# Kernel optimization log

Measured on AMD Instinct MI355X. Metric: run time of the kernel, lower is better.

Reference implementation:

```python
import jax, jax.numpy as jnp
import numpy as np


def setup_inputs() -> dict:
    key = jax.random.key(0)
    ks = jax.random.split(key, 7)
    B, N, D, A = 32, 128, 512, 512
    sD = 1.0 / np.sqrt(D)
    sA = 1.0 / np.sqrt(A)
    return {
        "x": jax.random.normal(ks[0], (B, N, D), dtype=jnp.float32),
        "W1": jax.random.normal(ks[1], (A, D), dtype=jnp.float32) * sD,
        "b1": jax.random.normal(ks[2], (A,), dtype=jnp.float32) * sD,
        "W2": jax.random.normal(ks[3], (A, D), dtype=jnp.float32) * sD,
        "b2": jax.random.normal(ks[4], (A,), dtype=jnp.float32) * sD,
        "Wout": jax.random.normal(ks[5], (A,), dtype=jnp.float32) * sA,
        "bout": jax.random.normal(ks[6], (1,), dtype=jnp.float32) * sA,
    }


def reference(x, W1, b1, W2, b2, Wout, bout):
    # x: (B, N, D)
    x1 = jnp.einsum('bnd,ad->bna', x, W1) + b1  # mlp1 -> (B, N, A)
    x2 = jnp.einsum('bnd,ad->bna', x, W2) + b2  # mlp2 -> (B, N, A)
    # outer broadcast add: x1.unsqueeze(1) + x2.unsqueeze(2) -> (B, N, N, A)
    s = x1[:, None, :, :] + x2[:, :, None, :]
    # include_root=False: drop ROOT row along dim 1 -> (B, N-1, N, A)
    s = s[:, 1:, :, :]
    s = jnp.tanh(s)
    # out linear A -> 1, then squeeze -> (B, N-1, N)
    return jnp.einsum('bija,a->bij', s, Wout) + bout[0]
```

## Files before the change

kernel.cpp:

```cpp
#include <hip/hip_runtime.h>
#include <hip/hip_bf16.h>

#define B_ 32
#define N_ 128
#define D_ 512
#define A_ 512
#define R_ (B_*N_)
#define OC 1024
#define CEXP 2.8853900817779268f

typedef __attribute__((ext_vector_type(8))) short  frag_ab;
typedef __attribute__((ext_vector_type(4))) float  frag_cd;

__device__ inline unsigned pack2bf(float a, float b) {
    unsigned ua = __builtin_bit_cast(unsigned, a) + 0x8000u;
    unsigned ub = __builtin_bit_cast(unsigned, b) + 0x8000u;
    return __builtin_amdgcn_perm(ub, ua, 0x07060302);
}
__device__ inline float bf2f_lo(unsigned u){ return __builtin_bit_cast(float, u << 16); }
__device__ inline float bf2f_hi(unsigned u){ return __builtin_bit_cast(float, u & 0xffff0000u); }

__global__ __launch_bounds__(256) void k0_cvt(
    const float* __restrict__ X, const float* __restrict__ W1,
    const float* __restrict__ W2,
    unsigned short* __restrict__ Xb, unsigned short* __restrict__ W1b,
    unsigned short* __restrict__ W2b)
{
    const int NX = R_*D_/8, NW = A_*D_/8;
    int i = blockIdx.x*256 + threadIdx.x;
    const float* src; unsigned short* dst; int off;
    if (i < NX)            { src = X;  dst = Xb;  off = i; }
    else if (i < NX+NW)    { src = W1; dst = W1b; off = i-NX; }
    else if (i < NX+2*NW)  { src = W2; dst = W2b; off = i-NX-NW; }
    else return;
    float4 a = ((const float4*)src)[off*2];
    float4 c = ((const float4*)src)[off*2+1];
    uint4 o;
    o.x = pack2bf(a.x,a.y); o.y = pack2bf(a.z,a.w);
    o.z = pack2bf(c.x,c.y); o.w = pack2bf(c.z,c.w);
    ((uint4*)dst)[off] = o;
}

#define BK1 64
#define LDK 68

__global__ __launch_bounds__(256) void k1_mfma(
    const unsigned short* __restrict__ Xb,
    const unsigned short* __restrict__ W1b, const float* __restrict__ b1,
    const unsigned short* __restrict__ W2b, const float* __restrict__ b2,
    unsigned short* __restrict__ Yb)
{
    __shared__ unsigned short As[2][64*LDK];
    __shared__ unsigned short Bs[2][64*LDK];

    const int t = threadIdx.x, lane = t&63, wid = t>>6;
    const int wr = wid>>1, wc = wid&1;
    const int row0 = blockIdx.x*64, col0 = blockIdx.y*64;
    const unsigned short* Wb = (col0 < A_) ? W1b : W2b;
    const float* bb = (col0 < A_) ? b1 : b2;
    const int wrow0 = col0 & (A_-1);

    const int srow = t>>3;
    const int scol = (t&7)*8;

    frag_cd acc[2][2];
#pragma unroll
    for (int i=0;i<2;++i)
#pragma unroll
        for (int j=0;j<2;++j) acc[i][j] = frag_cd{0.f,0.f,0.f,0.f};

    const int fr = lane&15, g8 = (lane>>4)*8;

    uint4 ra[2], rb[2];
#pragma unroll
    for (int q=0;q<2;++q){
        int r = q*32 + srow;
        ra[q] = *(const uint4*)&Xb[(size_t)(row0 +r)*D_ + scol];
        rb[q] = *(const uint4*)&Wb[(size_t)(wrow0+r)*D_ + scol];
    }
#pragma unroll
    for (int q=0;q<2;++q){
        int r = q*32 + srow;
        *(uint4*)&As[0][r*LDK + scol] = ra[q];
        *(uint4*)&Bs[0][r*LDK + scol] = rb[q];
    }
    __syncthreads();

#pragma unroll
    for (int s=0; s<8; ++s) {
        const int cur = s&1;
        if (s<7) {
            const int k0 = (s+1)*BK1;
#pragma unroll
            for (int q=0;q<2;++q){
                int r = q*32 + srow;
                ra[q] = *(const uint4*)&Xb[(size_t)(row0 +r)*D_ + k0 + scol];
                rb[q] = *(const uint4*)&Wb[(size_t)(wrow0+r)*D_ + k0 + scol];
            }
        }
        frag_ab af[2][2], bf[2][2];
#pragma unroll
        for (int fi=0;fi<2;++fi)
#pragma unroll
            for (int ks=0;ks<2;++ks) {
                af[fi][ks] = *(const frag_ab*)&As[cur][(wr*32+fi*16+fr)*LDK + ks*32 + g8];
                bf[fi][ks] = *(const frag_ab*)&Bs[cur][(wc*32+fi*16+fr)*LDK + ks*32 + g8];
            }
#pragma unroll
        for (int ks=0;ks<2;++ks)
#pragma unroll
            for (int fi=0;fi<2;++fi)
#pragma unroll
                for (int fj=0;fj<2;++fj)
                    acc[fi][fj] = __builtin_amdgcn_mfma_f32_16x16x32_bf16(
                        af[fi][ks], bf[fj][ks], acc[fi][fj], 0, 0, 0);
        if (s<7) {
#pragma unroll
            for (int q=0;q<2;++q){
                int r = q*32 + srow;
                *(uint4*)&As[cur^1][r*LDK + scol] = ra[q];
                *(uint4*)&Bs[cur^1][r*LDK + scol] = rb[q];
            }
        }
        __syncthreads();
    }

#pragma unroll
    for (int fi=0;fi<2;++fi){
        const int rr = row0 + wr*32 + fi*16 + (lane>>4)*4;
#pragma unroll
        for (int fj=0;fj<2;++fj){
            const int cc = col0 + wc*32 + fj*16 + (lane&15);
            const float bias = bb[cc & (A_-1)];
#pragma unroll
            for (int r=0;r<4;++r){
                float e = __builtin_amdgcn_exp2f(CEXP*(acc[fi][fj][r] + bias));
                Yb[(size_t)(rr+r)*OC + cc] =
                    (unsigned short)((__builtin_bit_cast(unsigned, e) + 0x8000u) >> 16);
            }
        }
    }
}

#define ACH 128
#define LDA2 (ACH+4)

__global__ __launch_bounds__(256) void k2_tanh(
    const unsigned short* __restrict__ Yb,
    const float* __restrict__ Wout, const float* __restrict__ bout,
    float* __restrict__ out)
{
    __shared__ float e1s[32][LDA2];
    __shared__ float e2s[16][LDA2];
    __shared__ float wo[A_];
    __shared__ float wsum_s[4];

    const int t  = threadIdx.x;
    const int jt = blockIdx.x;
    const int it = blockIdx.y;
    const int b  = blockIdx.z;

    float wsacc = 0.f;
    for (int k=t; k<A_; k+=256){ float w = Wout[k]; wo[k] = w; wsacc += w; }
#pragma unroll
    for (int off=32; off>=1; off>>=1) wsacc += __shfl_down(wsacc, off, 64);
    if ((t&63)==0) wsum_s[t>>6] = wsacc;

    const unsigned short* yb = Yb + (size_t)b*N_*OC;
    const int sr = t>>4;
    const int sc = (t&15)*8;

    uint4 p1a = *(const uint4*)&yb[(size_t)(jt*32 + sr     )*OC + sc];
    uint4 p1b = *(const uint4*)&yb[(size_t)(jt*32 + sr + 16)*OC + sc];
    int i2c = it*16 + sr + 1; if (i2c > 127) i2c = 127;
    uint4 p2  = *(const uint4*)&yb[(size_t)i2c*OC + A_ + sc];
    {
        uint4 v = p1a;
        *(float4*)&e1s[sr][sc]   = float4{bf2f_lo(v.x),bf2f_hi(v.x),bf2f_lo(v.y),bf2f_hi(v.y)};
        *(float4*)&e1s[sr][sc+4] = float4{bf2f_lo(v.z),bf2f_hi(v.z),bf2f_lo(v.w),bf2f_hi(v.w)};
        v = p1b;
        *(float4*)&e1s[sr+16][sc]   = float4{bf2f_lo(v.x),bf2f_hi(v.x),bf2f_lo(v.y),bf2f_hi(v.y)};
        *(float4*)&e1s[sr+16][sc+4] = float4{bf2f_lo(v.z),bf2f_hi(v.z),bf2f_lo(v.w),bf2f_hi(v.w)};
        v = p2;
        *(float4*)&e2s[sr][sc]   = float4{bf2f_lo(v.x),bf2f_hi(v.x),bf2f_lo(v.y),bf2f_hi(v.y)};
        *(float4*)&e2s[sr][sc+4] = float4{bf2f_lo(v.z),bf2f_hi(v.z),bf2f_lo(v.w),bf2f_hi(v.w)};
    }
    __syncthreads();

    const int jl = t&15, il = t>>4;
    float a00 = 0.f, a01 = 0.f;

#pragma unroll
    for (int ch=0; ch<4; ++ch) {
        if (ch<3) {
            const int a0n = (ch+1)*ACH;
            p1a = *(const uint4*)&yb[(size_t)(jt*32 + sr     )*OC + a0n + sc];
            p1b = *(const uint4*)&yb[(size_t)(jt*32 + sr + 16)*OC + a0n + sc];
            p2  = *(const uint4*)&yb[(size_t)i2c*OC + A_ + a0n + sc];
        }
        const int a0 = ch*ACH;
#pragma unroll 4
        for (int c=0; c<ACH; c+=4) {
            float4 u0 = *(const float4*)&e1s[jl     ][c];
            float4 u1 = *(const float4*)&e1s[jl + 16][c];
            float4 v0 = *(const float4*)&e2s[il     ][c];
            float4 w  = *(const float4*)&wo[a0 + c];
            a00 += w.x * __builtin_amdgcn_rcpf(fmaf(u0.x, v0.x, 1.f));
            a01 += w.x * __builtin_amdgcn_rcpf(fmaf(u1.x, v0.x, 1.f));
            a00 += w.y * __builtin_amdgcn_rcpf(fmaf(u0.y, v0.y, 1.f));
            a01 += w.y * __builtin_amdgcn_rcpf(fmaf(u1.y, v0.y, 1.f));
            a00 += w.z * __builtin_amdgcn_rcpf(fmaf(u0.z, v0.z, 1.f));
            a01 += w.z * __builtin_amdgcn_rcpf(fmaf(u1.z, v0.z, 1.f));
            a00 += w.w * __builtin_amdgcn_rcpf(fmaf(u0.w, v0.w, 1.f));
            a01 += w.w * __builtin_amdgcn_rcpf(fmaf(u1.w, v0.w, 1.f));
        }
        if (ch<3) {
            __syncthreads();
            uint4 v = p1a;
            *(float4*)&e1s[sr][sc]   = float4{bf2f_lo(v.x),bf2f_hi(v.x),bf2f_lo(v.y),bf2f_hi(v.y)};
            *(float4*)&e1s[sr][sc+4] = float4{bf2f_lo(v.z),bf2f_hi(v.z),bf2f_lo(v.w),bf2f_hi(v.w)};
            v = p1b;
            *(float4*)&e1s[sr+16][sc]   = float4{bf2f_lo(v.x),bf2f_hi(v.x),bf2f_lo(v.y),bf2f_hi(v.y)};
            *(float4*)&e1s[sr+16][sc+4] = float4{bf2f_lo(v.z),bf2f_hi(v.z),bf2f_lo(v.w),bf2f_hi(v.w)};
            v = p2;
            *(float4*)&e2s[sr][sc]   = float4{bf2f_lo(v.x),bf2f_hi(v.x),bf2f_lo(v.y),bf2f_hi(v.y)};
            *(float4*)&e2s[sr][sc+4] = float4{bf2f_lo(v.z),bf2f_hi(v.z),bf2f_lo(v.w),bf2f_hi(v.w)};
            __syncthreads();
        }
    }

    const float wsum = wsum_s[0] + wsum_s[1] + wsum_s[2] + wsum_s[3];
    const float bo   = bout[0];
    const int i0 = it*16 + il;
    const int j0 = jt*32 + jl;

    if (i0 < 127) {
        out[((size_t)(b*127) + i0) * 128 + j0     ] = wsum - 2.f*a00 + bo;
        out[((size_t)(b*127) + i0) * 128 + j0 + 16] = wsum - 2.f*a01 + bo;
    }
}

extern "C" void kernel_launch(void* const* d_in, const int* in_sizes, int n_in,
                              void* d_out, int out_size, void* d_ws, size_t ws_size,
                              hipStream_t stream) {
    const float* x    = (const float*)d_in[0];
    const float* W1   = (const float*)d_in[1];
    const float* b1   = (const float*)d_in[2];
    const float* W2   = (const float*)d_in[3];
    const float* b2   = (const float*)d_in[4];
    const float* Wout = (const float*)d_in[5];
    const float* bout = (const float*)d_in[6];
    float* out = (float*)d_out;

    char* ws = (char*)d_ws;
    unsigned short* Yb  = (unsigned short*)ws;
    unsigned short* Xb  = (unsigned short*)(ws + (8u<<20));
    unsigned short* W1b = (unsigned short*)(ws + (12u<<20));
    unsigned short* W2b = (unsigned short*)(ws + (12u<<20) + (1u<<19));

    k0_cvt<<<1280, 256, 0, stream>>>(x, W1, W2, Xb, W1b, W2b);

    dim3 g1(R_/64, OC/64);
    k1_mfma<<<g1, 256, 0, stream>>>(Xb, W1b, b1, W2b, b2, Yb);

    dim3 g2(4, 8, B_);
    k2_tanh<<<g2, 256, 0, stream>>>(Yb, Wout, bout, out);
}
```

Before: 115.6 us.

## Enlarge GEMM tiles to 32x32 MFMA and split tanh reduction across A halves

The projection GEMM moves from 64x64 tiles with 16x16x32 MFMA to 128x128 tiles with 32x32x16 MFMA and a K step of 32, raising data reuse per block. The tanh kernel now gives each thread a 2x2 output tile so loaded values are reused across more outputs. Pairs of reciprocals are merged into one rcp via the identity w1/r + w2/s = (w1*s + w2*r)/(r*s). The A dimension is split across two blocks whose partial sums are combined with atomicAdd into an output zeroed by a memset. This adds launch, memset and atomic overhead, makes float summation order nondeterministic, and the merged reciprocal risks overflow of r*s.

```diff
diff --git a/kernel.cpp b/kernel.cpp
--- a/kernel.cpp
+++ b/kernel.cpp
@@ -9,8 +9,8 @@
 #define OC 1024
 #define CEXP 2.8853900817779268f
 
-typedef __attribute__((ext_vector_type(8))) short  frag_ab;
-typedef __attribute__((ext_vector_type(4))) float  frag_cd;
+typedef __attribute__((ext_vector_type(8)))  short frag_ab;
+typedef __attribute__((ext_vector_type(16))) float frag_c;
 
 __device__ inline unsigned pack2bf(float a, float b) {
     unsigned ua = __builtin_bit_cast(unsigned, a) + 0x8000u;
@@ -19,6 +19,10 @@
 }
 __device__ inline float bf2f_lo(unsigned u){ return __builtin_bit_cast(float, u << 16); }
 __device__ inline float bf2f_hi(unsigned u){ return __builtin_bit_cast(float, u & 0xffff0000u); }
+__device__ inline void wr8(float* dst, uint4 v) {
+    *(float4*)dst     = float4{bf2f_lo(v.x),bf2f_hi(v.x),bf2f_lo(v.y),bf2f_hi(v.y)};
+    *(float4*)(dst+4) = float4{bf2f_lo(v.z),bf2f_hi(v.z),bf2f_lo(v.w),bf2f_hi(v.w)};
+}
 
 __global__ __launch_bounds__(256) void k0_cvt(
     const float* __restrict__ X, const float* __restrict__ W1,
@@ -41,8 +45,7 @@
     ((uint4*)dst)[off] = o;
 }
 
-#define BK1 64
-#define LDK 68
+#define LDK1 36
 
 __global__ __launch_bounds__(256) void k1_mfma(
     const unsigned short* __restrict__ Xb,
@@ -50,193 +53,198 @@
     const unsigned short* __restrict__ W2b, const float* __restrict__ b2,
     unsigned short* __restrict__ Yb)
 {
-    __shared__ unsigned short As[2][64*LDK];
-    __shared__ unsigned short Bs[2][64*LDK];
+    __shared__ unsigned short As[2][128*LDK1];
+    __shared__ unsigned short Bs[2][128*LDK1];
 
     const int t = threadIdx.x, lane = t&63, wid = t>>6;
     const int wr = wid>>1, wc = wid&1;
-    const int row0 = blockIdx.x*64, col0 = blockIdx.y*64;
+    const int row0 = blockIdx.x*128, col0 = blockIdx.y*128;
     const unsigned short* Wb = (col0 < A_) ? W1b : W2b;
     const float* bb = (col0 < A_) ? b1 : b2;
     const int wrow0 = col0 & (A_-1);
 
-    const int srow = t>>3;
-    const int scol = (t&7)*8;
-
-    frag_cd acc[2][2];
+    const int srow = t>>1;
+    const int scol = (t&1)*16;
+
+    frag_c acc[2][2];
 #pragma unroll
     for (int i=0;i<2;++i)
 #pragma unroll
-        for (int j=0;j<2;++j) acc[i][j] = frag_cd{0.f,0.f,0.f,0.f};
-
-    const int fr = lane&15, g8 = (lane>>4)*8;
-
-    uint4 ra[2], rb[2];
-#pragma unroll
-    for (int q=0;q<2;++q){
-        int r = q*32 + srow;
-        ra[q] = *(const uint4*)&Xb[(size_t)(row0 +r)*D_ + scol];
-        rb[q] = *(const uint4*)&Wb[(size_t)(wrow0+r)*D_ + scol];
-    }
-#pragma unroll
-    for (int q=0;q<2;++q){
-        int r = q*32 + srow;
-        *(uint4*)&As[0][r*LDK + scol] = ra[q];
-        *(uint4*)&Bs[0][r*LDK + scol] = rb[q];
-    }
-    __syncthreads();
-
-#pragma unroll
-    for (int s=0; s<8; ++s) {
-        const int cur = s&1;
-        if (s<7) {
-            const int k0 = (s+1)*BK1;
-#pragma unroll
-            for (int q=0;q<2;++q){
-                int r = q*32 + srow;
-                ra[q] = *(const uint4*)&Xb[(size_t)(row0 +r)*D_ + k0 + scol];
-                rb[q] = *(const uint4*)&Wb[(size_t)(wrow0+r)*D_ + k0 + scol];
-            }
+        for (int j=0;j<2;++j)
+#pragma unroll
+            for (int r=0;r<16;++r) acc[i][j][r] = 0.f;
+
+    const int fr = lane & 31;
+    const int ko = (lane >> 5) * 8;
+
+    {
+        const unsigned short* px = &Xb[(size_t)(row0 +srow)*D_ + scol];
+        const unsigned short* pw = &Wb[(size_t)(wrow0+srow)*D_ + scol];
+        uint4 a0 = *(const uint4*)px, a1 = *(const uint4*)(px+8);
+        uint4 b0 = *(const uint4*)pw, b1v = *(const uint4*)(pw+8);
+        *(uint4*)&As[0][srow*LDK1 + scol]     = a0;
+        *(uint4*)&As[0][srow*LDK1 + scol + 8] = a1;
+        *(uint4*)&Bs[0][srow*LDK1 + scol]     = b0;
+        *(uint4*)&Bs[0][srow*LDK1 + scol + 8] = b1v;
+    }
+    __syncthreads();
+
+#pragma unroll
+    for (int s = 0; s < 16; ++s) {
+        const int cur = s & 1;
+        uint4 a0, a1, b0, b1v;
+        if (s < 15) {
+            const int k0 = (s+1)*32;
+            const unsigned short* px = &Xb[(size_t)(row0 +srow)*D_ + k0 + scol];
+            const unsigned short* pw = &Wb[(size_t)(wrow0+srow)*D_ + k0 + scol];
+            a0 = *(const uint4*)px; a1 = *(const uint4*)(px+8);
+            b0 = *(const uint4*)pw; b1v = *(const uint4*)(pw+8);
         }
         frag_ab af[2][2], bf[2][2];
 #pragma unroll
-        for (int fi=0;fi<2;++fi)
-#pragma unroll
-            for (int ks=0;ks<2;++ks) {
-                af[fi][ks] = *(const frag_ab*)&As[cur][(wr*32+fi*16+fr)*LDK + ks*32 + g8];
-                bf[fi][ks] = *(const frag_ab*)&Bs[cur][(wc*32+fi*16+fr)*LDK + ks*32 + g8];
+        for (int mt=0; mt<2; ++mt)
+#pragma unroll
+            for (int ks=0; ks<2; ++ks) {
+                af[mt][ks] = *(const frag_ab*)&As[cur][(wr*64+mt*32+fr)*LDK1 + ks*16 + ko];
+                bf[mt][ks] = *(const frag_ab*)&Bs[cur][(wc*64+mt*32+fr)*LDK1 + ks*16 + ko];
             }
 #pragma unroll
-        for (int ks=0;ks<2;++ks)
-#pragma unroll
-            for (int fi=0;fi<2;++fi)
-#pragma unroll
-                for (int fj=0;fj<2;++fj)
-                    acc[fi][fj] = __builtin_amdgcn_mfma_f32_16x16x32_bf16(
-                        af[fi][ks], bf[fj][ks], acc[fi][fj], 0, 0, 0);
-        if (s<7) {
-#pragma unroll
-            for (int q=0;q<2;++q){
-                int r = q*32 + srow;
-                *(uint4*)&As[cur^1][r*LDK + scol] = ra[q];
-                *(uint4*)&Bs[cur^1][r*LDK + scol] = rb[q];
-            }
+        for (int ks=0; ks<2; ++ks)
+#pragma unroll
+            for (int mt=0; mt<2; ++mt)
+#pragma unroll
+                for (int nt=0; nt<2; ++nt)
+                    acc[mt][nt] = __builtin_amdgcn_mfma_f32_32x32x16_bf16(
+                        af[mt][ks], bf[nt][ks], acc[mt][nt], 0, 0, 0);
+        if (s < 15) {
+            *(uint4*)&As[cur^1][srow*LDK1 + scol]     = a0;
+            *(uint4*)&As[cur^1][srow*LDK1 + scol + 8] = a1;
+            *(uint4*)&Bs[cur^1][srow*LDK1 + scol]     = b0;
+            *(uint4*)&Bs[cur^1][srow*LDK1 + scol + 8] = b1v;
         }
         __syncthreads();
     }
 
 #pragma unroll
-    for (int fi=0;fi<2;++fi){
-        const int rr = row0 + wr*32 + fi*16 + (lane>>4)*4;
-#pragma unroll
-        for (int fj=0;fj<2;++fj){
-            const int cc = col0 + wc*32 + fj*16 + (lane&15);
+    for (int mt=0; mt<2; ++mt) {
+        const int rbase = row0 + wr*64 + mt*32 + 4*(lane>>5);
+#pragma unroll
+        for (int nt=0; nt<2; ++nt) {
+            const int cc = col0 + wc*64 + nt*32 + (lane&31);
             const float bias = bb[cc & (A_-1)];
 #pragma unroll
-            for (int r=0;r<4;++r){
-                float e = __builtin_amdgcn_exp2f(CEXP*(acc[fi][fj][r] + bias));
-                Yb[(size_t)(rr+r)*OC + cc] =
+            for (int r=0; r<16; ++r) {
+                const int rr = rbase + (r&3) + 8*(r>>2);
+                float e = __builtin_amdgcn_exp2f(CEXP*(acc[mt][nt][r] + bias));
+                Yb[(size_t)rr*OC + cc] =
                     (unsigned short)((__builtin_bit_cast(unsigned, e) + 0x8000u) >> 16);
             }
         }
     }
 }
 
-#define ACH 128
-#define LDA2 (ACH+4)
+#define ACH2 128
+#define LD2 (ACH2+4)
 
 __global__ __launch_bounds__(256) void k2_tanh(
     const unsigned short* __restrict__ Yb,
     const float* __restrict__ Wout, const float* __restrict__ bout,
     float* __restrict__ out)
 {
-    __shared__ float e1s[32][LDA2];
-    __shared__ float e2s[16][LDA2];
-    __shared__ float wo[A_];
+    __shared__ float e1s[32][LD2];
+    __shared__ float e2s[32][LD2];
+    __shared__ float wo[256];
     __shared__ float wsum_s[4];
 
     const int t  = threadIdx.x;
-    const int jt = blockIdx.x;
-    const int it = blockIdx.y;
-    const int b  = blockIdx.z;
-
-    float wsacc = 0.f;
-    for (int k=t; k<A_; k+=256){ float w = Wout[k]; wo[k] = w; wsacc += w; }
-#pragma unroll
-    for (int off=32; off>=1; off>>=1) wsacc += __shfl_down(wsacc, off, 64);
-    if ((t&63)==0) wsum_s[t>>6] = wsacc;
+    const int jt = blockIdx.x, it = blockIdx.y;
+    const int b  = blockIdx.z >> 1, ah = blockIdx.z & 1;
+    const int abase = ah << 8;
+
+    {
+        float w = Wout[abase + t];
+        wo[t] = w;
+#pragma unroll
+        for (int off=32; off>=1; off>>=1) w += __shfl_down(w, off, 64);
+        if ((t&63)==0) wsum_s[t>>6] = w;
+    }
 
     const unsigned short* yb = Yb + (size_t)b*N_*OC;
-    const int sr = t>>4;
-    const int sc = (t&15)*8;
-
-    uint4 p1a = *(const uint4*)&yb[(size_t)(jt*32 + sr     )*OC + sc];
-    uint4 p1b = *(const uint4*)&yb[(size_t)(jt*32 + sr + 16)*OC + sc];
-    int i2c = it*16 + sr + 1; if (i2c > 127) i2c = 127;
-    uint4 p2  = *(const uint4*)&yb[(size_t)i2c*OC + A_ + sc];
+    const int sr = t>>4, sc = (t&15)*8;
+    int i2a = it*32 + sr + 1;  if (i2a > 127) i2a = 127;
+    int i2b = it*32 + sr + 17; if (i2b > 127) i2b = 127;
+    const size_t o1a = (size_t)(jt*32+sr   )*OC + abase + sc;
+    const size_t o1b = (size_t)(jt*32+sr+16)*OC + abase + sc;
+    const size_t o2a = (size_t)i2a*OC + A_ + abase + sc;
+    const size_t o2b = (size_t)i2b*OC + A_ + abase + sc;
+
     {
-        uint4 v = p1a;
-        *(float4*)&e1s[sr][sc]   = float4{bf2f_lo(v.x),bf2f_hi(v.x),bf2f_lo(v.y),bf2f_hi(v.y)};
-        *(float4*)&e1s[sr][sc+4] = float4{bf2f_lo(v.z),bf2f_hi(v.z),bf2f_lo(v.w),bf2f_hi(v.w)};
-        v = p1b;
-        *(float4*)&e1s[sr+16][sc]   = float4{bf2f_lo(v.x),bf2f_hi(v.x),bf2f_lo(v.y),bf2f_hi(v.y)};
-        *(float4*)&e1s[sr+16][sc+4] = float4{bf2f_lo(v.z),bf2f_hi(v.z),bf2f_lo(v.w),bf2f_hi(v.w)};
-        v = p2;
-        *(float4*)&e2s[sr][sc]   = float4{bf2f_lo(v.x),bf2f_hi(v.x),bf2f_lo(v.y),bf2f_hi(v.y)};
-        *(float4*)&e2s[sr][sc+4] = float4{bf2f_lo(v.z),bf2f_hi(v.z),bf2f_lo(v.w),bf2f_hi(v.w)};
-    }
-    __syncthreads();
+        uint4 v1a = *(const uint4*)&yb[o1a];
+        uint4 v1b = *(const uint4*)&yb[o1b];
+        uint4 v2a = *(const uint4*)&yb[o2a];
+        uint4 v2b = *(const uint4*)&yb[o2b];
+        wr8(&e1s[sr][sc], v1a); wr8(&e1s[sr+16][sc], v1b);
+        wr8(&e2s[sr][sc], v2a); wr8(&e2s[sr+16][sc], v2b);
+    }
+    __syncthreads();
+
+    uint4 n1a = *(const uint4*)&yb[o1a + ACH2];
+    uint4 n1b = *(const uint4*)&yb[o1b + ACH2];
+    uint4 n2a = *(const uint4*)&yb[o2a + ACH2];
+    uint4 n2b = *(const uint4*)&yb[o2b + ACH2];
 
     const int jl = t&15, il = t>>4;
-    float a00 = 0.f, a01 = 0.f;
-
-#pragma unroll
-    for (int ch=0; ch<4; ++ch) {
-        if (ch<3) {
-            const int a0n = (ch+1)*ACH;
-            p1a = *(const uint4*)&yb[(size_t)(jt*32 + sr     )*OC + a0n + sc];
-            p1b = *(const uint4*)&yb[(size_t)(jt*32 + sr + 16)*OC + a0n + sc];
-            p2  = *(const uint4*)&yb[(size_t)i2c*OC + A_ + a0n + sc];
-        }
-        const int a0 = ch*ACH;
+    float a00=0.f, a01=0.f, a10=0.f, a11=0.f;
+
 #pragma unroll 4
-        for (int c=0; c<ACH; c+=4) {
-            float4 u0 = *(const float4*)&e1s[jl     ][c];
-            float4 u1 = *(const float4*)&e1s[jl + 16][c];
-            float4 v0 = *(const float4*)&e2s[il     ][c];
-            float4 w  = *(const float4*)&wo[a0 + c];
-            a00 += w.x * __builtin_amdgcn_rcpf(fmaf(u0.x, v0.x, 1.f));
-            a01 += w.x * __builtin_amdgcn_rcpf(fmaf(u1.x, v0.x, 1.f));
-            a00 += w.y * __builtin_amdgcn_rcpf(fmaf(u0.y, v0.y, 1.f));
-            a01 += w.y * __builtin_amdgcn_rcpf(fmaf(u1.y, v0.y, 1.f));
-            a00 += w.z * __builtin_amdgcn_rcpf(fmaf(u0.z, v0.z, 1.f));
-            a01 += w.z * __builtin_amdgcn_rcpf(fmaf(u1.z, v0.z, 1.f));
-            a00 += w.w * __builtin_amdgcn_rcpf(fmaf(u0.w, v0.w, 1.f));
-            a01 += w.w * __builtin_amdgcn_rcpf(fmaf(u1.w, v0.w, 1.f));
-        }
-        if (ch<3) {
-            __syncthreads();
-            uint4 v = p1a;
-            *(float4*)&e1s[sr][sc]   = float4{bf2f_lo(v.x),bf2f_hi(v.x),bf2f_lo(v.y),bf2f_hi(v.y)};
-            *(float4*)&e1s[sr][sc+4] = float4{bf2f_lo(v.z),bf2f_hi(v.z),bf2f_lo(v.w),bf2f_hi(v.w)};
-            v = p1b;
-            *(float4*)&e1s[sr+16][sc]   = float4{bf2f_lo(v.x),bf2f_hi(v.x),bf2f_lo(v.y),bf2f_hi(v.y)};
-            *(float4*)&e1s[sr+16][sc+4] = float4{bf2f_lo(v.z),bf2f_hi(v.z),bf2f_lo(v.w),bf2f_hi(v.w)};
-            v = p2;
-            *(float4*)&e2s[sr][sc]   = float4{bf2f_lo(v.x),bf2f_hi(v.x),bf2f_lo(v.y),bf2f_hi(v.y)};
-            *(float4*)&e2s[sr][sc+4] = float4{bf2f_lo(v.z),bf2f_hi(v.z),bf2f_lo(v.w),bf2f_hi(v.w)};
-            __syncthreads();
-        }
-    }
-
-    const float wsum = wsum_s[0] + wsum_s[1] + wsum_s[2] + wsum_s[3];
-    const float bo   = bout[0];
-    const int i0 = it*16 + il;
-    const int j0 = jt*32 + jl;
-
+    for (int c=0; c<ACH2; c+=2) {
+        float2 u0 = *(const float2*)&e1s[jl   ][c];
+        float2 u1 = *(const float2*)&e1s[jl+16][c];
+        float2 v0 = *(const float2*)&e2s[il   ][c];
+        float2 v1 = *(const float2*)&e2s[il+16][c];
+        float2 w  = *(const float2*)&wo[c];
+        { float r=fmaf(u0.x,v0.x,1.f), s=fmaf(u0.y,v0.y,1.f);
+          a00 = fmaf(fmaf(w.x,s,w.y*r), __builtin_amdgcn_rcpf(r*s), a00); }
+        { float r=fmaf(u1.x,v0.x,1.f), s=fmaf(u1.y,v0.y,1.f);
+          a01 = fmaf(fmaf(w.x,s,w.y*r), __builtin_amdgcn_rcpf(r*s), a01); }
+        { float r=fmaf(u0.x,v1.x,1.f), s=fmaf(u0.y,v1.y,1.f);
+          a10 = fmaf(fmaf(w.x,s,w.y*r), __builtin_amdgcn_rcpf(r*s), a10); }
+        { float r=fmaf(u1.x,v1.x,1.f), s=fmaf(u1.y,v1.y,1.f);
+          a11 = fmaf(fmaf(w.x,s,w.y*r), __builtin_amdgcn_rcpf(r*s), a11); }
+    }
+    __syncthreads();
+    wr8(&e1s[sr][sc], n1a); wr8(&e1s[sr+16][sc], n1b);
+    wr8(&e2s[sr][sc], n2a); wr8(&e2s[sr+16][sc], n2b);
+    __syncthreads();
+
+#pragma unroll 4
+    for (int c=0; c<ACH2; c+=2) {
+        float2 u0 = *(const float2*)&e1s[jl   ][c];
+        float2 u1 = *(const float2*)&e1s[jl+16][c];
+        float2 v0 = *(const float2*)&e2s[il   ][c];
+        float2 v1 = *(const float2*)&e2s[il+16][c];
+        float2 w  = *(const float2*)&wo[ACH2 + c];
+        { float r=fmaf(u0.x,v0.x,1.f), s=fmaf(u0.y,v0.y,1.f);
+          a00 = fmaf(fmaf(w.x,s,w.y*r), __builtin_amdgcn_rcpf(r*s), a00); }
+        { float r=fmaf(u1.x,v0.x,1.f), s=fmaf(u1.y,v0.y,1.f);
+          a01 = fmaf(fmaf(w.x,s,w.y*r), __builtin_amdgcn_rcpf(r*s), a01); }
+        { float r=fmaf(u0.x,v1.x,1.f), s=fmaf(u0.y,v1.y,1.f);
+          a10 = fmaf(fmaf(w.x,s,w.y*r), __builtin_amdgcn_rcpf(r*s), a10); }
+        { float r=fmaf(u1.x,v1.x,1.f), s=fmaf(u1.y,v1.y,1.f);
+          a11 = fmaf(fmaf(w.x,s,w.y*r), __builtin_amdgcn_rcpf(r*s), a11); }
+    }
+
+    const float wsum = wsum_s[0]+wsum_s[1]+wsum_s[2]+wsum_s[3];
+    const float base = wsum + (ah ? 0.f : bout[0]);
+    const int i0 = it*32 + il, j0 = jt*32 + jl;
+    float* ob = out + (size_t)b*127*128;
     if (i0 < 127) {
-        out[((size_t)(b*127) + i0) * 128 + j0     ] = wsum - 2.f*a00 + bo;
-        out[((size_t)(b*127) + i0) * 128 + j0 + 16] = wsum - 2.f*a01 + bo;
+        atomicAdd(&ob[i0*128 + j0     ], base - 2.f*a00);
+        atomicAdd(&ob[i0*128 + j0 + 16], base - 2.f*a01);
+    }
+    if (i0 + 16 < 127) {
+        atomicAdd(&ob[(i0+16)*128 + j0     ], base - 2.f*a10);
+        atomicAdd(&ob[(i0+16)*128 + j0 + 16], base - 2.f*a11);
     }
 }
 
@@ -260,9 +268,11 @@
 
     k0_cvt<<<1280, 256, 0, stream>>>(x, W1, W2, Xb, W1b, W2b);
 
-    dim3 g1(R_/64, OC/64);
+    dim3 g1(R_/128, OC/128);
     k1_mfma<<<g1, 256, 0, stream>>>(Xb, W1b, b1, W2b, b2, Yb);
 
-    dim3 g2(4, 8, B_);
+    hipMemsetAsync(d_out, 0, (size_t)out_size*sizeof(float), stream);
+
+    dim3 g2(4, 4, 2*B_);
     k2_tanh<<<g2, 256, 0, stream>>>(Yb, Wout, bout, out);
 }
```

Result: no change. 114.5 us (-0.9%).
